# Performance work log

Measured on AMD Instinct MI355X. Metric: run time of the kernel, lower is better.

## Reference

```python
import jax, jax.numpy as jnp
import numpy as np

CHANNEL = 512
INTER = CHANNEL // 2


def setup_inputs() -> dict:
    key = jax.random.key(0)
    ks = jax.random.split(key, 7)
    b, c, h, w = 8, CHANNEL, 64, 64
    q = jax.random.normal(ks[0], (b, c, h, w), dtype=jnp.float32)
    k = jax.random.normal(ks[1], (b, c, h, w), dtype=jnp.float32)
    v = jax.random.normal(ks[2], (b, c, h, w), dtype=jnp.float32)
    # 1x1 conv weights, no bias: (out_ch, in_ch)
    s_in = 1.0 / np.sqrt(c)
    s_int = 1.0 / np.sqrt(INTER)
    W_phi = jax.random.uniform(ks[3], (INTER, c), jnp.float32, -s_in, s_in)
    W_theta = jax.random.uniform(ks[4], (INTER, c), jnp.float32, -s_in, s_in)
    W_g = jax.random.uniform(ks[5], (INTER, c), jnp.float32, -s_in, s_in)
    W_mask = jax.random.uniform(ks[6], (c, INTER), jnp.float32, -s_int, s_int)
    return {"q": q, "k": k, "v": v, "W_phi": W_phi, "W_theta": W_theta,
            "W_g": W_g, "W_mask": W_mask}


def reference(q, k, v, W_phi, W_theta, W_g, W_mask):
    b, c, h, w = q.shape
    inter = c // 2
    hw2 = (h * w) // 2  # quirk: conv output (b, c/2, h, w) is reshaped to (b, c, hw/2)
    # 1x1 convs as channel matmuls
    phi = jnp.einsum('oc,bchw->bohw', W_phi, q).reshape(b, c, hw2)        # (b, c, hw2)
    theta = jnp.einsum('oc,bchw->bohw', W_theta, k).reshape(b, c, hw2)    # (b, c, hw2)
    g = jnp.einsum('oc,bchw->bohw', W_g, v).reshape(b, c, hw2)            # (b, c, hw2)
    # scores: (b, hw2, c) @ (b, c, hw2) -> (b, hw2, hw2)
    scores = jnp.einsum('bcn,bcm->bnm', theta, phi)
    attn = jax.nn.softmax(scores, axis=1)  # torch Softmax(dim=1): over rows
    # (b, hw2, hw2) @ (b, hw2, c) -> (b, hw2, c)
    y = jnp.einsum('bnm,bcn->bmc', attn, g)
    y = jnp.transpose(y, (0, 2, 1)).reshape(b, inter, h, w)
    mask = jnp.einsum('oc,bchw->bohw', W_mask, y)
    return mask + q + v
```

## Files before the change

kernel.cpp:

```cpp
#include <hip/hip_runtime.h>
#include <hip/hip_bf16.h>
#include <math.h>

typedef __hip_bfloat16 hbf16;
typedef __attribute__((ext_vector_type(8))) short short8;
typedef __attribute__((ext_vector_type(4))) float f32x4;

static const long QS = 2097152;

__device__ __forceinline__ unsigned short f2bf(float f) {
    hbf16 h = __float2bfloat16(f);
    return *reinterpret_cast<unsigned short*>(&h);
}
__device__ __forceinline__ float bf2f(unsigned short u) {
    unsigned x = ((unsigned)u) << 16;
    return __uint_as_float(x);
}
__device__ __forceinline__ unsigned pk2(float a, float b) {
    return (unsigned)f2bf(a) | ((unsigned)f2bf(b) << 16);
}

__device__ __forceinline__ void gload16(const void* g, void* l) {
    __builtin_amdgcn_global_load_lds(
        (const __attribute__((address_space(1))) void*)g,
        (__attribute__((address_space(3))) void*)l, 16, 0, 0);
}

template <int R>
__device__ __forceinline__ void stage_direct(const short* P, int ld, int row0,
                                             long koff, short* Ls) {
    const int tid = threadIdx.x;
    const int w = tid >> 6, lane = tid & 63;
    const int lrow = lane >> 3;
    const int s = lane & 7;
#pragma unroll
    for (int j = 0; j < R / 32; ++j) {
        int rowbase = w * (R / 4) + j * 8;
        int r = rowbase + lrow;
        int g = s ^ (r & 7);
        const short* ga = P + (long)(row0 + r) * ld + koff + g * 8;
        gload16(ga, Ls + rowbase * 64);
    }
}

template <int R>
__device__ __forceinline__ void stage_trans(const float* X, int sld, int row0,
                                            int k0, short* Ls) {
    const int tid = threadIdx.x;
    constexpr int L2R = (R == 128) ? 7 : 6;
#pragma unroll
    for (int j = 0; j < R / 32; ++j) {
        int idx = j * 256 + tid;
        int r = idx & (R - 1);
        int c = idx >> L2R;
        long base = (long)(k0 + c * 8) * sld + row0 + r;
        float f[8];
#pragma unroll
        for (int jj = 0; jj < 8; ++jj) f[jj] = X[base + (long)jj * sld];
        uint4 pkv;
        pkv.x = pk2(f[0], f[1]);
        pkv.y = pk2(f[2], f[3]);
        pkv.z = pk2(f[4], f[5]);
        pkv.w = pk2(f[6], f[7]);
        int s = c ^ (r & 7);
        *reinterpret_cast<uint4*>(Ls + r * 64 + s * 8) = pkv;
    }
}

#define EPI_BF 0
#define EPI_YT 1
#define EPI_OUT 2

template <int TM, int TN, bool TRA, bool TRB, int EPI>
__global__ __launch_bounds__(256) void mm(
    const short* __restrict__ A, const float* __restrict__ Af,
    const short* __restrict__ B, const float* __restrict__ Bf,
    void* __restrict__ C, const float* __restrict__ Rq, const float* __restrict__ Rv,
    int K, int lda, int ldb, int ldc, int kmask, int kshift, long kpanel,
    long bsA, long bsB, long bsC, long bsR)
{
    __shared__ __align__(16) short As[TM * 64];
    __shared__ __align__(16) short Bs[TN * 64];

    const int tid = threadIdx.x;
    const int w = tid >> 6, lane = tid & 63;
    const int quad = lane >> 4, l16 = lane & 15;
    const int m0 = blockIdx.y * TM;
    const int n0 = blockIdx.x * TN;
    const int bz = blockIdx.z;

    if constexpr (TRA) Af += (long)bz * bsA; else A += (long)bz * bsA;
    if constexpr (TRB) Bf += (long)bz * bsB; else B += (long)bz * bsB;
    const long cb = (long)bz * bsC;
    if constexpr (EPI == EPI_OUT) { Rq += (long)bz * bsR; Rv += (long)bz * bsR; }

    constexpr int WM = TM / 2;
    constexpr int MT = WM / 16;
    const int wm = (w & 1) * WM;
    const int wn = (w >> 1) * 64;

    f32x4 acc[MT][4];
#pragma unroll
    for (int i = 0; i < MT; ++i)
#pragma unroll
        for (int j = 0; j < 4; ++j) acc[i][j] = (f32x4){0.f, 0.f, 0.f, 0.f};

    for (int k0 = 0; k0 < K; k0 += 64) {
        __syncthreads();
        long koff = (long)(k0 & kmask) + (long)(k0 >> kshift) * kpanel;
        if constexpr (TRA) stage_trans<TM>(Af, lda, m0, k0, As);
        else               stage_direct<TM>(A, lda, m0, koff, As);
        if constexpr (TRB) stage_trans<TN>(Bf, ldb, n0, k0, Bs);
        else               stage_direct<TN>(B, ldb, n0, koff, Bs);
        __syncthreads();

#pragma unroll
        for (int ks = 0; ks < 2; ++ks) {
            short8 af[MT], bfr[4];
#pragma unroll
            for (int mt = 0; mt < MT; ++mt) {
                int r = wm + mt * 16 + l16;
                int s = (ks * 4 + quad) ^ (r & 7);
                af[mt] = *reinterpret_cast<const short8*>(&As[r * 64 + s * 8]);
            }
#pragma unroll
            for (int nt = 0; nt < 4; ++nt) {
                int r = wn + nt * 16 + l16;
                int s = (ks * 4 + quad) ^ (r & 7);
                bfr[nt] = *reinterpret_cast<const short8*>(&Bs[r * 64 + s * 8]);
            }
#pragma unroll
            for (int mt = 0; mt < MT; ++mt)
#pragma unroll
                for (int nt = 0; nt < 4; ++nt)
                    acc[mt][nt] = __builtin_amdgcn_mfma_f32_16x16x32_bf16(
                        af[mt], bfr[nt], acc[mt][nt], 0, 0, 0);
        }
    }

#pragma unroll
    for (int mt = 0; mt < MT; ++mt)
#pragma unroll
        for (int nt = 0; nt < 4; ++nt)
#pragma unroll
            for (int reg = 0; reg < 4; ++reg) {
                int gr = m0 + wm + mt * 16 + quad * 4 + reg;
                int gc = n0 + wn + nt * 16 + l16;
                float vacc = acc[mt][nt][reg];
                if constexpr (EPI == EPI_BF) {
                    ((short*)C)[cb + (long)gr * ldc + gc] = (short)f2bf(vacc);
                } else if constexpr (EPI == EPI_YT) {
                    long a = (long)gc * 256 + (long)(gr & 1) * 524288 + (gr >> 1);
                    ((short*)C)[cb + a] = (short)f2bf(vacc);
                } else {
                    long a = (long)gr * 4096 + gc;
                    ((float*)C)[cb + a] = vacc + Rq[a] + Rv[a];
                }
            }
}

__global__ __launch_bounds__(256) void softmax_row(short* __restrict__ T) {
    const int row = blockIdx.x;
    const int tid = threadIdx.x;
    const int w = tid >> 6, lane = tid & 63;
    __shared__ float red[8];

    uint4 u = *reinterpret_cast<const uint4*>(&T[(long)row * 2048 + tid * 8]);
    float f[8];
    f[0] = bf2f((unsigned short)(u.x & 0xffff)); f[1] = bf2f((unsigned short)(u.x >> 16));
    f[2] = bf2f((unsigned short)(u.y & 0xffff)); f[3] = bf2f((unsigned short)(u.y >> 16));
    f[4] = bf2f((unsigned short)(u.z & 0xffff)); f[5] = bf2f((unsigned short)(u.z >> 16));
    f[6] = bf2f((unsigned short)(u.w & 0xffff)); f[7] = bf2f((unsigned short)(u.w >> 16));

    float m = f[0];
#pragma unroll
    for (int j = 1; j < 8; ++j) m = fmaxf(m, f[j]);
    for (int o = 32; o > 0; o >>= 1) m = fmaxf(m, __shfl_down(m, o));
    if (lane == 0) red[w] = m;
    __syncthreads();
    float M = fmaxf(fmaxf(red[0], red[1]), fmaxf(red[2], red[3]));

    float e[8], s = 0.f;
#pragma unroll
    for (int j = 0; j < 8; ++j) { e[j] = __expf(f[j] - M); s += e[j]; }
    for (int o = 32; o > 0; o >>= 1) s += __shfl_down(s, o);
    if (lane == 0) red[4 + w] = s;
    __syncthreads();
    float invL = 1.0f / (red[4] + red[5] + red[6] + red[7]);

    uint4 ov;
    ov.x = pk2(e[0] * invL, e[1] * invL);
    ov.y = pk2(e[2] * invL, e[3] * invL);
    ov.z = pk2(e[4] * invL, e[5] * invL);
    ov.w = pk2(e[6] * invL, e[7] * invL);
    *reinterpret_cast<uint4*>(&T[(long)row * 2048 + tid * 8]) = ov;
}

__global__ __launch_bounds__(256) void cast_w(
    const float* __restrict__ a, const float* __restrict__ b,
    const float* __restrict__ c, const float* __restrict__ d,
    short* __restrict__ W)
{
    const float* S[4] = {a, b, c, d};
    int sel = blockIdx.y;
    int i = (blockIdx.x * 256 + threadIdx.x) * 4;
    float4 f = *reinterpret_cast<const float4*>(&S[sel][i]);
    uint2 o;
    o.x = pk2(f.x, f.y);
    o.y = pk2(f.z, f.w);
    *reinterpret_cast<uint2*>(&W[sel * 131072 + i]) = o;
}

extern "C" void kernel_launch(void* const* d_in, const int* in_sizes, int n_in,
                              void* d_out, int out_size, void* d_ws, size_t ws_size,
                              hipStream_t stream)
{
    const float* q    = (const float*)d_in[0];
    const float* kk   = (const float*)d_in[1];
    const float* v    = (const float*)d_in[2];
    const float* Wphi = (const float*)d_in[3];
    const float* Wth  = (const float*)d_in[4];
    const float* Wg   = (const float*)d_in[5];
    const float* Wm   = (const float*)d_in[6];
    float* out = (float*)d_out;
    dim3 blk(256);

    const long PB = 8388608;
    long ws_shorts = (long)(ws_size / 2);
    int NB = (int)((ws_shorts - 524288) / PB);
    if (NB > 8) NB = 8;
    if (NB < 1) NB = 1;

    short* Wb   = (short*)d_ws;
    short* Phi  = Wb + 524288;
    short* Th   = Phi + (long)NB * 1048576;
    short* Gr   = Th + (long)NB * 1048576;
    short* T    = Gr + (long)NB * 1048576;
    short* YtvT = T + (long)NB * 4194304;
    const short* WbPhi = Wb;
    const short* WbTh  = Wb + 131072;
    const short* WbG   = Wb + 262144;
    const short* WbM   = Wb + 393216;

    const int LIN_M = 0x3FFFFFFF, LIN_S = 30;

    cast_w<<<dim3(128, 4), blk, 0, stream>>>(Wphi, Wth, Wg, Wm, Wb);

    for (int b0 = 0; b0 < 8; b0 += NB) {
        int nb = 8 - b0 < NB ? 8 - b0 : NB;
        const float* qb = q + (long)b0 * QS;
        const float* kb = kk + (long)b0 * QS;
        const float* vb = v + (long)b0 * QS;

        mm<128, 128, true, false, EPI_BF><<<dim3(2, 32, nb), blk, 0, stream>>>(
            nullptr, qb, WbPhi, nullptr, Phi, nullptr, nullptr,
            512, 4096, 512, 256, LIN_M, LIN_S, 0,
            QS, 0, 1048576, 0);
        mm<128, 128, true, false, EPI_BF><<<dim3(2, 32, nb), blk, 0, stream>>>(
            nullptr, kb, WbTh, nullptr, Th, nullptr, nullptr,
            512, 4096, 512, 256, LIN_M, LIN_S, 0,
            QS, 0, 1048576, 0);
        mm<128, 128, false, true, EPI_BF><<<dim3(32, 2, nb), blk, 0, stream>>>(
            WbG, nullptr, nullptr, vb, Gr, nullptr, nullptr,
            512, 512, 4096, 4096, LIN_M, LIN_S, 0,
            0, QS, 1048576, 0);

        mm<128, 128, false, false, EPI_BF><<<dim3(16, 16, nb), blk, 0, stream>>>(
            Phi, nullptr, Th, nullptr, T, nullptr, nullptr,
            512, 256, 256, 2048, 255, 8, 524288,
            1048576, 1048576, 4194304, 0);

        softmax_row<<<dim3(2048 * nb), blk, 0, stream>>>(T);

        mm<64, 128, false, false, EPI_YT><<<dim3(16, 8, nb), blk, 0, stream>>>(
            Gr, nullptr, T, nullptr, YtvT, nullptr, nullptr,
            2048, 2048, 2048, 256, LIN_M, LIN_S, 0,
            1048576, 4194304, 1048576, 0);

        mm<128, 128, false, false, EPI_OUT><<<dim3(32, 4, nb), blk, 0, stream>>>(
            WbM, nullptr, YtvT, nullptr, out + (long)b0 * QS, qb, vb,
            256, 256, 256, 4096, LIN_M, LIN_S, 0,
            0, 1048576, QS, QS);
    }
}
```

Baseline: 424.9 us.

## Prefetch transposed fp32 tiles into registers and merge phi/theta projections

```diff
diff --git a/kernel.cpp b/kernel.cpp
--- a/kernel.cpp
+++ b/kernel.cpp
@@ -44,8 +44,8 @@
 }
 
 template <int R>
-__device__ __forceinline__ void stage_trans(const float* X, int sld, int row0,
-                                            int k0, short* Ls) {
+__device__ __forceinline__ void trans_load(const float* X, int sld, int row0,
+                                           int k0, float (&f)[R / 32][8]) {
     const int tid = threadIdx.x;
     constexpr int L2R = (R == 128) ? 7 : 6;
 #pragma unroll
@@ -54,14 +54,25 @@
         int r = idx & (R - 1);
         int c = idx >> L2R;
         long base = (long)(k0 + c * 8) * sld + row0 + r;
-        float f[8];
-#pragma unroll
-        for (int jj = 0; jj < 8; ++jj) f[jj] = X[base + (long)jj * sld];
+#pragma unroll
+        for (int jj = 0; jj < 8; ++jj) f[j][jj] = X[base + (long)jj * sld];
+    }
+}
+
+template <int R>
+__device__ __forceinline__ void trans_write(const float (&f)[R / 32][8], short* Ls) {
+    const int tid = threadIdx.x;
+    constexpr int L2R = (R == 128) ? 7 : 6;
+#pragma unroll
+    for (int j = 0; j < R / 32; ++j) {
+        int idx = j * 256 + tid;
+        int r = idx & (R - 1);
+        int c = idx >> L2R;
         uint4 pkv;
-        pkv.x = pk2(f[0], f[1]);
-        pkv.y = pk2(f[2], f[3]);
-        pkv.z = pk2(f[4], f[5]);
-        pkv.w = pk2(f[6], f[7]);
+        pkv.x = pk2(f[j][0], f[j][1]);
+        pkv.y = pk2(f[j][2], f[j][3]);
+        pkv.z = pk2(f[j][4], f[j][5]);
+        pkv.w = pk2(f[j][6], f[j][7]);
         int s = c ^ (r & 7);
         *reinterpret_cast<uint4*>(Ls + r * 64 + s * 8) = pkv;
     }
@@ -71,11 +82,13 @@
 #define EPI_YT 1
 #define EPI_OUT 2
 
-template <int TM, int TN, bool TRA, bool TRB, int EPI>
+template <int TM, int TN, bool TRA, bool TRB, int EPI, bool DUAL>
 __global__ __launch_bounds__(256) void mm(
     const short* __restrict__ A, const float* __restrict__ Af,
-    const short* __restrict__ B, const float* __restrict__ Bf,
-    void* __restrict__ C, const float* __restrict__ Rq, const float* __restrict__ Rv,
+    const float* __restrict__ Af2,
+    const short* __restrict__ B, long selB, const float* __restrict__ Bf,
+    void* __restrict__ C, long selC,
+    const float* __restrict__ Rq, const float* __restrict__ Rv,
     int K, int lda, int ldb, int ldc, int kmask, int kshift, long kpanel,
     long bsA, long bsB, long bsC, long bsR)
 {
@@ -87,11 +100,14 @@
     const int quad = lane >> 4, l16 = lane & 15;
     const int m0 = blockIdx.y * TM;
     const int n0 = blockIdx.x * TN;
-    const int bz = blockIdx.z;
-
-    if constexpr (TRA) Af += (long)bz * bsA; else A += (long)bz * bsA;
-    if constexpr (TRB) Bf += (long)bz * bsB; else B += (long)bz * bsB;
-    const long cb = (long)bz * bsC;
+    int bz = blockIdx.z, sel = 0;
+    if constexpr (DUAL) { sel = bz & 1; bz >>= 1; }
+
+    if constexpr (TRA) Af = ((DUAL && sel) ? Af2 : Af) + (long)bz * bsA;
+    else               A += (long)bz * bsA;
+    if constexpr (TRB) Bf += (long)bz * bsB;
+    else               B += (long)bz * bsB + (long)sel * selB;
+    const long cb = (long)bz * bsC + (long)sel * selC;
     if constexpr (EPI == EPI_OUT) { Rq += (long)bz * bsR; Rv += (long)bz * bsR; }
 
     constexpr int WM = TM / 2;
@@ -105,14 +121,26 @@
 #pragma unroll
         for (int j = 0; j < 4; ++j) acc[i][j] = (f32x4){0.f, 0.f, 0.f, 0.f};
 
+    constexpr int NA = TRA ? TM / 32 : 1;
+    constexpr int NB_ = TRB ? TN / 32 : 1;
+    float fa[NA][8];
+    float fb[NB_][8];
+    if constexpr (TRA) trans_load<TM>(Af, lda, m0, 0, fa);
+    if constexpr (TRB) trans_load<TN>(Bf, ldb, n0, 0, fb);
+
     for (int k0 = 0; k0 < K; k0 += 64) {
         __syncthreads();
         long koff = (long)(k0 & kmask) + (long)(k0 >> kshift) * kpanel;
-        if constexpr (TRA) stage_trans<TM>(Af, lda, m0, k0, As);
+        if constexpr (TRA) trans_write<TM>(fa, As);
         else               stage_direct<TM>(A, lda, m0, koff, As);
-        if constexpr (TRB) stage_trans<TN>(Bf, ldb, n0, k0, Bs);
+        if constexpr (TRB) trans_write<TN>(fb, Bs);
         else               stage_direct<TN>(B, ldb, n0, koff, Bs);
         __syncthreads();
+
+        if (k0 + 64 < K) {
+            if constexpr (TRA) trans_load<TM>(Af, lda, m0, k0 + 64, fa);
+            if constexpr (TRB) trans_load<TN>(Bf, ldb, n0, k0 + 64, fb);
+        }
 
 #pragma unroll
         for (int ks = 0; ks < 2; ++ks) {
@@ -238,7 +266,6 @@
     short* T    = Gr + (long)NB * 1048576;
     short* YtvT = T + (long)NB * 4194304;
     const short* WbPhi = Wb;
-    const short* WbTh  = Wb + 131072;
     const short* WbG   = Wb + 262144;
     const short* WbM   = Wb + 393216;
 
@@ -252,33 +279,31 @@
         const float* kb = kk + (long)b0 * QS;
         const float* vb = v + (long)b0 * QS;
 
-        mm<128, 128, true, false, EPI_BF><<<dim3(2, 32, nb), blk, 0, stream>>>(
-            nullptr, qb, WbPhi, nullptr, Phi, nullptr, nullptr,
+        mm<64, 128, true, false, EPI_BF, true><<<dim3(2, 64, nb * 2), blk, 0, stream>>>(
+            nullptr, qb, kb, WbPhi, 131072, nullptr, Phi, (long)NB * 1048576,
+            nullptr, nullptr,
             512, 4096, 512, 256, LIN_M, LIN_S, 0,
             QS, 0, 1048576, 0);
-        mm<128, 128, true, false, EPI_BF><<<dim3(2, 32, nb), blk, 0, stream>>>(
-            nullptr, kb, WbTh, nullptr, Th, nullptr, nullptr,
-            512, 4096, 512, 256, LIN_M, LIN_S, 0,
-            QS, 0, 1048576, 0);
-        mm<128, 128, false, true, EPI_BF><<<dim3(32, 2, nb), blk, 0, stream>>>(
-            WbG, nullptr, nullptr, vb, Gr, nullptr, nullptr,
+
+        mm<64, 128, false, true, EPI_BF, false><<<dim3(32, 4, nb), blk, 0, stream>>>(
+            WbG, nullptr, nullptr, nullptr, 0, vb, Gr, 0, nullptr, nullptr,
             512, 512, 4096, 4096, LIN_M, LIN_S, 0,
             0, QS, 1048576, 0);
 
-        mm<128, 128, false, false, EPI_BF><<<dim3(16, 16, nb), blk, 0, stream>>>(
-            Phi, nullptr, Th, nullptr, T, nullptr, nullptr,
+        mm<128, 128, false, false, EPI_BF, false><<<dim3(16, 16, nb), blk, 0, stream>>>(
+            Phi, nullptr, nullptr, Th, 0, nullptr, T, 0, nullptr, nullptr,
             512, 256, 256, 2048, 255, 8, 524288,
             1048576, 1048576, 4194304, 0);
 
         softmax_row<<<dim3(2048 * nb), blk, 0, stream>>>(T);
 
-        mm<64, 128, false, false, EPI_YT><<<dim3(16, 8, nb), blk, 0, stream>>>(
-            Gr, nullptr, T, nullptr, YtvT, nullptr, nullptr,
+        mm<64, 128, false, false, EPI_YT, false><<<dim3(16, 8, nb), blk, 0, stream>>>(
+            Gr, nullptr, nullptr, T, 0, nullptr, YtvT, 0, nullptr, nullptr,
             2048, 2048, 2048, 256, LIN_M, LIN_S, 0,
             1048576, 4194304, 1048576, 0);
 
-        mm<128, 128, false, false, EPI_OUT><<<dim3(32, 4, nb), blk, 0, stream>>>(
-            WbM, nullptr, YtvT, nullptr, out + (long)b0 * QS, qb, vb,
+        mm<128, 128, false, false, EPI_OUT, false><<<dim3(32, 4, nb), blk, 0, stream>>>(
+            WbM, nullptr, nullptr, YtvT, 0, nullptr, out + (long)b0 * QS, 0, qb, vb,
             256, 256, 256, 4096, LIN_M, LIN_S, 0,
             0, 1048576, QS, QS);
     }
```

After: 425.5 us. Within noise of the previous version (+0.1%).

## Add dedicated fp32-input conv GEMM with async LDS staging and dual phi/theta launch

Applied to the files above, without the earlier changes.

```diff
diff --git a/kernel.cpp b/kernel.cpp
--- a/kernel.cpp
+++ b/kernel.cpp
@@ -24,6 +24,113 @@
     __builtin_amdgcn_global_load_lds(
         (const __attribute__((address_space(1))) void*)g,
         (__attribute__((address_space(3))) void*)l, 16, 0, 0);
+}
+
+template <bool PTM, bool DUAL>
+__global__ __launch_bounds__(256) void convmm(
+    const float* __restrict__ X0, const float* __restrict__ X1,
+    const short* __restrict__ W, long selW,
+    short* __restrict__ C, long selC,
+    int ldc, long bsX, long bsC)
+{
+    __shared__ __align__(16) float Lf[32 * 256];
+    __shared__ __align__(16) short Ps[256 * 40];
+    __shared__ __align__(16) short Ws[64 * 40];
+
+    const int tid = threadIdx.x;
+    const int w = tid >> 6, lane = tid & 63;
+    const int quad = lane >> 4, l16 = lane & 15;
+
+    int bz = blockIdx.z, sel = 0;
+    if constexpr (DUAL) { sel = bz & 1; bz >>= 1; }
+
+    const int p0 = (PTM ? blockIdx.y : blockIdx.x) * 256;
+    const int w0 = (PTM ? blockIdx.x : blockIdx.y) * 64;
+
+    const float* X = ((DUAL && sel) ? X1 : X0) + (long)bz * bsX;
+    const short* Wp = W + (long)sel * selW;
+    short* Cp = C + (long)bz * bsC + (long)sel * selC;
+
+    const int wr = tid >> 2, wc = tid & 3;
+    short8 wreg;
+
+    f32x4 acc[4][4];
+#pragma unroll
+    for (int i = 0; i < 4; ++i)
+#pragma unroll
+        for (int j = 0; j < 4; ++j) acc[i][j] = (f32x4){0.f, 0.f, 0.f, 0.f};
+
+    auto issueX = [&](int k0) {
+#pragma unroll
+        for (int i = 0; i < 8; ++i) {
+            int e = i * 1024 + tid * 4;
+            int kc = e >> 8, p = e & 255;
+            gload16(X + (long)(k0 + kc) * 4096 + p0 + p,
+                    Lf + i * 1024 + w * 256);
+        }
+    };
+    auto loadW = [&](int k0) {
+        wreg = *reinterpret_cast<const short8*>(
+            &Wp[(long)(w0 + wr) * 512 + k0 + wc * 8]);
+    };
+
+    issueX(0);
+    loadW(0);
+
+    for (int k0 = 0; k0 < 512; k0 += 32) {
+        __syncthreads();
+
+#pragma unroll
+        for (int u = 0; u < 4; ++u) {
+            float f[8];
+#pragma unroll
+            for (int j = 0; j < 8; ++j) f[j] = Lf[(u * 8 + j) * 256 + tid];
+            uint4 pk;
+            pk.x = pk2(f[0], f[1]);
+            pk.y = pk2(f[2], f[3]);
+            pk.z = pk2(f[4], f[5]);
+            pk.w = pk2(f[6], f[7]);
+            *reinterpret_cast<uint4*>(&Ps[tid * 40 + u * 8]) = pk;
+        }
+        *reinterpret_cast<short8*>(&Ws[wr * 40 + wc * 8]) = wreg;
+
+        __syncthreads();
+
+        if (k0 + 32 < 512) { issueX(k0 + 32); loadW(k0 + 32); }
+
+        short8 af[4], bf[4];
+#pragma unroll
+        for (int mt = 0; mt < 4; ++mt) {
+            int r = PTM ? (w * 64 + mt * 16 + l16) : (mt * 16 + l16);
+            const short* base = PTM ? Ps : Ws;
+            af[mt] = *reinterpret_cast<const short8*>(&base[r * 40 + quad * 8]);
+        }
+#pragma unroll
+        for (int nt = 0; nt < 4; ++nt) {
+            int r = PTM ? (nt * 16 + l16) : (w * 64 + nt * 16 + l16);
+            const short* base = PTM ? Ws : Ps;
+            bf[nt] = *reinterpret_cast<const short8*>(&base[r * 40 + quad * 8]);
+        }
+#pragma unroll
+        for (int mt = 0; mt < 4; ++mt)
+#pragma unroll
+            for (int nt = 0; nt < 4; ++nt)
+                acc[mt][nt] = __builtin_amdgcn_mfma_f32_16x16x32_bf16(
+                    af[mt], bf[nt], acc[mt][nt], 0, 0, 0);
+    }
+
+#pragma unroll
+    for (int mt = 0; mt < 4; ++mt)
+#pragma unroll
+        for (int nt = 0; nt < 4; ++nt)
+#pragma unroll
+            for (int reg = 0; reg < 4; ++reg) {
+                int gr = (PTM ? (blockIdx.y * 256 + w * 64 + mt * 16)
+                              : (blockIdx.y * 64 + mt * 16)) + quad * 4 + reg;
+                int gc = (PTM ? (blockIdx.x * 64 + nt * 16)
+                              : (blockIdx.x * 256 + w * 64 + nt * 16)) + l16;
+                Cp[(long)gr * ldc + gc] = (short)f2bf(acc[mt][nt][reg]);
+            }
 }
 
 template <int R>
@@ -43,38 +150,13 @@
     }
 }
 
-template <int R>
-__device__ __forceinline__ void stage_trans(const float* X, int sld, int row0,
-                                            int k0, short* Ls) {
-    const int tid = threadIdx.x;
-    constexpr int L2R = (R == 128) ? 7 : 6;
-#pragma unroll
-    for (int j = 0; j < R / 32; ++j) {
-        int idx = j * 256 + tid;
-        int r = idx & (R - 1);
-        int c = idx >> L2R;
-        long base = (long)(k0 + c * 8) * sld + row0 + r;
-        float f[8];
-#pragma unroll
-        for (int jj = 0; jj < 8; ++jj) f[jj] = X[base + (long)jj * sld];
-        uint4 pkv;
-        pkv.x = pk2(f[0], f[1]);
-        pkv.y = pk2(f[2], f[3]);
-        pkv.z = pk2(f[4], f[5]);
-        pkv.w = pk2(f[6], f[7]);
-        int s = c ^ (r & 7);
-        *reinterpret_cast<uint4*>(Ls + r * 64 + s * 8) = pkv;
-    }
-}
-
 #define EPI_BF 0
 #define EPI_YT 1
 #define EPI_OUT 2
 
-template <int TM, int TN, bool TRA, bool TRB, int EPI>
+template <int TM, int TN, int EPI>
 __global__ __launch_bounds__(256) void mm(
-    const short* __restrict__ A, const float* __restrict__ Af,
-    const short* __restrict__ B, const float* __restrict__ Bf,
+    const short* __restrict__ A, const short* __restrict__ B,
     void* __restrict__ C, const float* __restrict__ Rq, const float* __restrict__ Rv,
     int K, int lda, int ldb, int ldc, int kmask, int kshift, long kpanel,
     long bsA, long bsB, long bsC, long bsR)
@@ -89,8 +171,8 @@
     const int n0 = blockIdx.x * TN;
     const int bz = blockIdx.z;
 
-    if constexpr (TRA) Af += (long)bz * bsA; else A += (long)bz * bsA;
-    if constexpr (TRB) Bf += (long)bz * bsB; else B += (long)bz * bsB;
+    A += (long)bz * bsA;
+    B += (long)bz * bsB;
     const long cb = (long)bz * bsC;
     if constexpr (EPI == EPI_OUT) { Rq += (long)bz * bsR; Rv += (long)bz * bsR; }
 
@@ -108,10 +190,8 @@
     for (int k0 = 0; k0 < K; k0 += 64) {
         __syncthreads();
         long koff = (long)(k0 & kmask) + (long)(k0 >> kshift) * kpanel;
-        if constexpr (TRA) stage_trans<TM>(Af, lda, m0, k0, As);
-        else               stage_direct<TM>(A, lda, m0, koff, As);
-        if constexpr (TRB) stage_trans<TN>(Bf, ldb, n0, k0, Bs);
-        else               stage_direct<TN>(B, ldb, n0, koff, Bs);
+        stage_direct<TM>(A, lda, m0, koff, As);
+        stage_direct<TN>(B, ldb, n0, koff, Bs);
         __syncthreads();
 
 #pragma unroll
@@ -238,7 +318,6 @@
     short* T    = Gr + (long)NB * 1048576;
     short* YtvT = T + (long)NB * 4194304;
     const short* WbPhi = Wb;
-    const short* WbTh  = Wb + 131072;
     const short* WbG   = Wb + 262144;
     const short* WbM   = Wb + 393216;
 
@@ -252,33 +331,28 @@
         const float* kb = kk + (long)b0 * QS;
         const float* vb = v + (long)b0 * QS;
 
-        mm<128, 128, true, false, EPI_BF><<<dim3(2, 32, nb), blk, 0, stream>>>(
-            nullptr, qb, WbPhi, nullptr, Phi, nullptr, nullptr,
-            512, 4096, 512, 256, LIN_M, LIN_S, 0,
-            QS, 0, 1048576, 0);
-        mm<128, 128, true, false, EPI_BF><<<dim3(2, 32, nb), blk, 0, stream>>>(
-            nullptr, kb, WbTh, nullptr, Th, nullptr, nullptr,
-            512, 4096, 512, 256, LIN_M, LIN_S, 0,
-            QS, 0, 1048576, 0);
-        mm<128, 128, false, true, EPI_BF><<<dim3(32, 2, nb), blk, 0, stream>>>(
-            WbG, nullptr, nullptr, vb, Gr, nullptr, nullptr,
-            512, 512, 4096, 4096, LIN_M, LIN_S, 0,
-            0, QS, 1048576, 0);
-
-        mm<128, 128, false, false, EPI_BF><<<dim3(16, 16, nb), blk, 0, stream>>>(
-            Phi, nullptr, Th, nullptr, T, nullptr, nullptr,
+        convmm<true, true><<<dim3(4, 16, nb * 2), blk, 0, stream>>>(
+            qb, kb, WbPhi, 131072, Phi, (long)NB * 1048576,
+            256, QS, 1048576);
+
+        convmm<false, false><<<dim3(16, 4, nb), blk, 0, stream>>>(
+            vb, nullptr, WbG, 0, Gr, 0,
+            4096, QS, 1048576);
+
+        mm<128, 128, EPI_BF><<<dim3(16, 16, nb), blk, 0, stream>>>(
+            Phi, Th, T, nullptr, nullptr,
             512, 256, 256, 2048, 255, 8, 524288,
             1048576, 1048576, 4194304, 0);
 
         softmax_row<<<dim3(2048 * nb), blk, 0, stream>>>(T);
 
-        mm<64, 128, false, false, EPI_YT><<<dim3(16, 8, nb), blk, 0, stream>>>(
-            Gr, nullptr, T, nullptr, YtvT, nullptr, nullptr,
+        mm<64, 128, EPI_YT><<<dim3(16, 8, nb), blk, 0, stream>>>(
+            Gr, T, YtvT, nullptr, nullptr,
             2048, 2048, 2048, 256, LIN_M, LIN_S, 0,
             1048576, 4194304, 1048576, 0);
 
-        mm<128, 128, false, false, EPI_OUT><<<dim3(32, 4, nb), blk, 0, stream>>>(
-            WbM, nullptr, YtvT, nullptr, out + (long)b0 * QS, qb, vb,
+        mm<128, 128, EPI_OUT><<<dim3(32, 4, nb), blk, 0, stream>>>(
+            WbM, YtvT, out + (long)b0 * QS, qb, vb,
             256, 256, 256, 4096, LIN_M, LIN_S, 0,
             0, 1048576, QS, QS);
     }
```

Result: slower. 450.5 us (+6.0%).
